# Kernel tuning notes

Hardware: AMD Instinct MI355X
Metric: run time of the kernel (lower is better)

Reference implementation:

```python
import jax, jax.numpy as jnp
import numpy as np

FIELD_DIMS = [26000] * 39
EMBED_DIM = 64
MLP_DIMS = [400, 400, 400]
BATCH = 16384
OFFSETS = jnp.asarray(np.concatenate(([0], np.cumsum(FIELD_DIMS)[:-1])), dtype=jnp.int32)
BN_INV = 1.0 / np.sqrt(1.0 + 1e-5)  # eval-mode BatchNorm1d: running_mean=0, running_var=1


def setup_inputs() -> dict:
    key = jax.random.key(0)
    ks = jax.random.split(key, 16)
    B, F, E = BATCH, len(FIELD_DIMS), EMBED_DIM
    V = sum(FIELD_DIMS)
    s = lambda k, shp, sc=0.05: (jax.random.normal(k, shp, jnp.float32) * sc)
    inp = {
        "x": jax.random.randint(ks[0], (B, F), 0, FIELD_DIMS[0], dtype=jnp.int32),
        "emb_table": s(ks[1], (V, E)),
        "lin_table": s(ks[2], (V, 1)),
        "lin_bias": jnp.zeros((1,), jnp.float32),
        "sparse_var": s(ks[3], (F, E), 0.1),
        "Wt": s(ks[4], (F, E, E)),  # per-field Linear weights, (out,in) layout
        "bt": jnp.zeros((F, E), jnp.float32),
    }
    dims = [F * E] + MLP_DIMS
    for i in range(3):
        inp[f"W{i+1}"] = s(ks[5 + i], (dims[i], dims[i + 1]))
        inp[f"b{i+1}"] = jnp.zeros((dims[i + 1],), jnp.float32)
        inp[f"g{i+1}"] = jnp.ones((dims[i + 1],), jnp.float32)
        inp[f"be{i+1}"] = jnp.zeros((dims[i + 1],), jnp.float32)
    inp["Wout"] = s(ks[9], (MLP_DIMS[-1], 1))
    inp["bout"] = jnp.zeros((1,), jnp.float32)
    return inp


def reference(x, emb_table, lin_table, lin_bias, sparse_var, Wt, bt,
              W1, b1, g1, be1, W2, b2, g2, be2, W3, b3, g3, be3, Wout, bout):
    B = x.shape[0]
    idx = x + OFFSETS[None, :]                       # (B, F) global vocab ids
    # sparse gate (detached in torch), eval-mode hard threshold mask
    sv = jax.nn.sigmoid(jax.lax.stop_gradient(sparse_var) * 15.0)
    sv = jnp.where(sv > 0.001, sv, 0.0)              # (F, E)
    embed_x = emb_table[idx] * sv                    # (B, F, E) gather + gate
    # per-field small Linear, batched as one einsum (torch: y = e @ W.T + b)
    trans = jnp.einsum('bfi,foi->bfo', embed_x, Wt) + bt  # (B, F, E)
    # FM second-order term
    sum_f = trans.sum(axis=1)                        # (B, E)
    fm = 0.5 * jnp.sum(sum_f * sum_f - (trans * trans).sum(axis=1),
                       axis=-1, keepdims=True)       # (B, 1)
    # first-order linear term
    lin = lin_table[idx].sum(axis=1) + lin_bias      # (B, 1)
    # MLP on flattened gated embeddings (Linear -> BN(eval) -> ReLU)
    h = embed_x.reshape(B, -1)
    for W, b, g, be in ((W1, b1, g1, be1), (W2, b2, g2, be2), (W3, b3, g3, be3)):
        h = jax.nn.relu((h @ W + b) * (BN_INV * g) + be)
    mlp = h @ Wout + bout                            # (B, 1)
    return jax.nn.sigmoid(jnp.squeeze(lin + fm + mlp, axis=1))  # (B,)
```

## Files before the change

kernel.cpp:

```cpp
#include <hip/hip_runtime.h>

#define BT 16384
#define NF 39
#define FD 26000

typedef unsigned short u16;
typedef unsigned int u32;
typedef short bf16x8 __attribute__((ext_vector_type(8)));
typedef float f32x4 __attribute__((ext_vector_type(4)));

__device__ __forceinline__ float bf2f(u16 h) {
  union { u32 u; float f; } v; v.u = ((u32)h) << 16; return v.f;
}
__device__ __forceinline__ u16 f2bf(float f) {
  union { float f; u32 u; } v; v.f = f;
  u32 r = v.u + 0x7fffu + ((v.u >> 16) & 1u);
  return (u16)(r >> 16);
}
__device__ __forceinline__ void gld16(const u16* g, u16* l) {
  __builtin_amdgcn_global_load_lds(
      (const __attribute__((address_space(1))) void*)g,
      (__attribute__((address_space(3))) void*)l, 16, 0, 0);
}

__global__ __launch_bounds__(256) void k_prep(
    const float* __restrict__ W1, u16* __restrict__ W1T,
    const float* __restrict__ W2, u16* __restrict__ W2T,
    const float* __restrict__ W3, u16* __restrict__ W3T,
    const float* __restrict__ Wt, u16* __restrict__ Wtb)
{
  int z = blockIdx.z;
  if (z == 3) {
    int idx = (blockIdx.y * 14 + blockIdx.x) * 256 + threadIdx.x;
    if (idx < NF * 4096) Wtb[idx] = f2bf(Wt[idx]);
    return;
  }
  const float* in = (z == 0) ? W1 : (z == 1) ? W2 : W3;
  u16* outp = (z == 0) ? W1T : (z == 1) ? W2T : W3T;
  int K = (z == 0) ? 2496 : 400;
  int Kpad = (z == 0) ? 2496 : 448;
  int r0 = blockIdx.y * 32, c0 = blockIdx.x * 32;
  if (r0 >= Kpad) return;
  __shared__ u16 t[32][33];
  int tx = threadIdx.x & 31, ty = threadIdx.x >> 5;
  for (int i = ty; i < 32; i += 8) {
    int r = r0 + i, c = c0 + tx;
    t[i][tx] = (r < K && c < 400) ? f2bf(in[(long)r * 400 + c]) : (u16)0;
  }
  __syncthreads();
  int r = r0 + tx;
  if (r < Kpad)
    for (int i = ty; i < 32; i += 8)
      outp[(long)(c0 + i) * Kpad + r] = t[tx][i];
}

__global__ __launch_bounds__(256) void k_embed(
    const int* __restrict__ x, const float* __restrict__ emb,
    const float* __restrict__ lin_table, const float* __restrict__ lin_bias,
    const float* __restrict__ sparse_var, const u16* __restrict__ Wtb,
    const float* __restrict__ bt, u16* __restrict__ h0, float* __restrict__ base)
{
  __shared__ u16                s_x[32 * NF];
  __shared__ float              s_sv[NF * 64];
  __shared__ float              s_bt[NF * 64];
  __shared__ __align__(16) u16  s_emb[2][32 * 72];
  __shared__ __align__(16) u16  s_wt[2][64 * 64];
  __shared__ float              s_fm[64];
  __shared__ float              s_lin[32];

  const int tid = threadIdx.x;
  const int b0 = blockIdx.x * 32;

  for (int i = tid; i < 32 * NF; i += 256) s_x[i] = (u16)x[b0 * NF + i];
  for (int i = tid; i < NF * 64; i += 256) {
    float v = sparse_var[i];
    float s = 1.0f / (1.0f + __expf(-15.0f * v));
    s_sv[i] = (s > 0.001f) ? s : 0.0f;
    s_bt[i] = bt[i];
  }
  __syncthreads();

  const int wave = tid >> 6, lane = tid & 63;
  const int quad = lane >> 4, c16 = lane & 15;
  const int mt = wave & 1, nh = wave >> 1;
  const int g_row = tid >> 3, g_c8 = (tid & 7) * 8;
  const int wrow = lane >> 3;
  const int wchk = (lane & 7) ^ wrow;

  float q[4] = {0.f, 0.f, 0.f, 0.f};
  float accS[2][4] = {{0.f,0.f,0.f,0.f},{0.f,0.f,0.f,0.f}};

  #pragma unroll
  for (int i = 0; i < 2; ++i) {
    int ii = wave * 2 + i;
    gld16(Wtb + (ii * 8 + wrow) * 64 + wchk * 8, &s_wt[0][ii * 512]);
  }
  {
    long gi = (long)((int)s_x[g_row * NF + 0]);
    float4 e0 = *(const float4*)&emb[gi * 64 + g_c8];
    float4 e1 = *(const float4*)&emb[gi * 64 + g_c8 + 4];
    union { uint4 v; u16 h[8]; } p;
    p.h[0] = f2bf(e0.x * s_sv[g_c8 + 0]);
    p.h[1] = f2bf(e0.y * s_sv[g_c8 + 1]);
    p.h[2] = f2bf(e0.z * s_sv[g_c8 + 2]);
    p.h[3] = f2bf(e0.w * s_sv[g_c8 + 3]);
    p.h[4] = f2bf(e1.x * s_sv[g_c8 + 4]);
    p.h[5] = f2bf(e1.y * s_sv[g_c8 + 5]);
    p.h[6] = f2bf(e1.z * s_sv[g_c8 + 6]);
    p.h[7] = f2bf(e1.w * s_sv[g_c8 + 7]);
    *(uint4*)&s_emb[0][g_row * 72 + g_c8] = p.v;
    *(uint4*)&h0[(long)(b0 + g_row) * 2496 + g_c8] = p.v;
  }
  __syncthreads();

  for (int f = 0; f < NF; ++f) {
    const int cur = f & 1, nxt = cur ^ 1;
    float4 e0, e1;
    const bool more = (f + 1) < NF;
    if (more) {
      #pragma unroll
      for (int i = 0; i < 2; ++i) {
        int ii = wave * 2 + i;
        gld16(Wtb + (f + 1) * 4096 + (ii * 8 + wrow) * 64 + wchk * 8,
              &s_wt[nxt][ii * 512]);
      }
      long gi = (long)((int)s_x[g_row * NF + f + 1] + (f + 1) * FD);
      e0 = *(const float4*)&emb[gi * 64 + g_c8];
      e1 = *(const float4*)&emb[gi * 64 + g_c8 + 4];
    }

    bf16x8 a0 = *(const bf16x8*)&s_emb[cur][(mt * 16 + c16) * 72 + quad * 8];
    bf16x8 a1 = *(const bf16x8*)&s_emb[cur][(mt * 16 + c16) * 72 + 32 + quad * 8];
    #pragma unroll
    for (int j = 0; j < 2; ++j) {
      int row = (nh * 2 + j) * 16 + c16;
      int pc0 = quad ^ (row & 7);
      int pc1 = (quad + 4) ^ (row & 7);
      bf16x8 bb0 = *(const bf16x8*)&s_wt[cur][row * 64 + pc0 * 8];
      bf16x8 bb1 = *(const bf16x8*)&s_wt[cur][row * 64 + pc1 * 8];
      f32x4 acc = {0.f, 0.f, 0.f, 0.f};
      acc = __builtin_amdgcn_mfma_f32_16x16x32_bf16(a0, bb0, acc, 0, 0, 0);
      acc = __builtin_amdgcn_mfma_f32_16x16x32_bf16(a1, bb1, acc, 0, 0, 0);
      float btv = s_bt[f * 64 + row];
      #pragma unroll
      for (int r = 0; r < 4; ++r) {
        float t = acc[r] + btv;
        accS[j][r] += t;
        q[r] += t * t;
      }
    }

    if (more) {
      union { uint4 v; u16 h[8]; } p;
      const float* sv = &s_sv[(f + 1) * 64 + g_c8];
      p.h[0] = f2bf(e0.x * sv[0]);
      p.h[1] = f2bf(e0.y * sv[1]);
      p.h[2] = f2bf(e0.z * sv[2]);
      p.h[3] = f2bf(e0.w * sv[3]);
      p.h[4] = f2bf(e1.x * sv[4]);
      p.h[5] = f2bf(e1.y * sv[5]);
      p.h[6] = f2bf(e1.z * sv[6]);
      p.h[7] = f2bf(e1.w * sv[7]);
      *(uint4*)&s_emb[nxt][g_row * 72 + g_c8] = p.v;
      *(uint4*)&h0[(long)(b0 + g_row) * 2496 + (f + 1) * 64 + g_c8] = p.v;
    }
    __syncthreads();
  }

  #pragma unroll
  for (int r = 0; r < 4; ++r) {
    float v = accS[0][r] * accS[0][r] + accS[1][r] * accS[1][r] - q[r];
    v += __shfl_xor(v, 1, 64);
    v += __shfl_xor(v, 2, 64);
    v += __shfl_xor(v, 4, 64);
    v += __shfl_xor(v, 8, 64);
    if (c16 == 0) s_fm[nh * 32 + mt * 16 + quad * 4 + r] = v;
  }
  {
    int row = tid >> 3, fi = tid & 7;
    float lv = 0.f;
    for (int f = fi; f < NF; f += 8)
      lv += lin_table[(int)s_x[row * NF + f] + f * FD];
    lv += __shfl_xor(lv, 1, 64);
    lv += __shfl_xor(lv, 2, 64);
    lv += __shfl_xor(lv, 4, 64);
    if (fi == 0) s_lin[row] = lv;
  }
  __syncthreads();
  if (tid < 32)
    base[b0 + tid] = s_lin[tid] + lin_bias[0]
                   + 0.5f * (s_fm[tid] + s_fm[32 + tid]);
}

__global__ __launch_bounds__(256) void k_gemm(
    const u16* __restrict__ A, int lda, const u16* __restrict__ Bt, int ldb,
    int kit, const float* __restrict__ bias, const float* __restrict__ g,
    const float* __restrict__ be, u16* __restrict__ C, int ldc)
{
  __shared__ __align__(16) u16 sA[128 * 64];
  __shared__ __align__(16) u16 sB[112 * 64];

  const int tid = threadIdx.x;
  int bid = blockIdx.x;
  int xcd = bid & 7;
  int j = bid >> 3;
  const int m0 = (xcd * 16 + (j >> 2)) * 128;
  const int n0 = (j & 3) * 112;

  const int wave = tid >> 6, lane = tid & 63;
  const int quad = lane >> 4, c16 = lane & 15;

  const int srow = lane >> 3;
  const int sclog = (lane & 7) ^ (srow & 7);
  const u16* gA = A + (long)m0 * lda + sclog * 8;
  const u16* gB = Bt + (long)n0 * ldb + sclog * 8;

  f32x4 acc[2][7];
  #pragma unroll
  for (int mtt = 0; mtt < 2; ++mtt)
    #pragma unroll
    for (int nt = 0; nt < 7; ++nt) acc[mtt][nt] = {0.f, 0.f, 0.f, 0.f};

  for (int kk = 0; kk < kit; ++kk) {
    const int k0 = kk * 64;
    #pragma unroll
    for (int it = 0; it < 4; ++it) {
      int s = wave * 4 + it;
      gld16(gA + (long)(s * 8 + srow) * lda + k0, &sA[s * 512]);
    }
    gld16(gB + (long)(wave * 8 + srow) * ldb + k0, &sB[wave * 512]);
    gld16(gB + (long)((wave + 4) * 8 + srow) * ldb + k0, &sB[(wave + 4) * 512]);
    gld16(gB + (long)((wave + 8) * 8 + srow) * ldb + k0, &sB[(wave + 8) * 512]);
    if (wave < 2)
      gld16(gB + (long)((wave + 12) * 8 + srow) * ldb + k0, &sB[(wave + 12) * 512]);
    __syncthreads();

    #pragma unroll
    for (int ks = 0; ks < 2; ++ks) {
      const int co = ((ks * 4 + quad) ^ (c16 & 7)) * 8;
      bf16x8 a0 = *(const bf16x8*)&sA[(wave * 32 + c16) * 64 + co];
      bf16x8 a1 = *(const bf16x8*)&sA[(wave * 32 + 16 + c16) * 64 + co];
      #pragma unroll
      for (int nt = 0; nt < 7; ++nt) {
        bf16x8 b = *(const bf16x8*)&sB[(nt * 16 + c16) * 64 + co];
        acc[0][nt] = __builtin_amdgcn_mfma_f32_16x16x32_bf16(a0, b, acc[0][nt], 0, 0, 0);
        acc[1][nt] = __builtin_amdgcn_mfma_f32_16x16x32_bf16(a1, b, acc[1][nt], 0, 0, 0);
      }
    }
    __syncthreads();
  }

  const float BN_INV = 0.9999950000374997f;
  #pragma unroll
  for (int nt = 0; nt < 7; ++nt) {
    int col = n0 + nt * 16 + c16;
    if (col < 400) {
      float bb = bias[col];
      float sc = BN_INV * g[col];
      float bv = be[col];
      #pragma unroll
      for (int mtt = 0; mtt < 2; ++mtt) {
        #pragma unroll
        for (int r = 0; r < 4; ++r) {
          int row = m0 + wave * 32 + mtt * 16 + quad * 4 + r;
          float y = (acc[mtt][nt][r] + bb) * sc + bv;
          y = fmaxf(y, 0.f);
          C[(long)row * ldc + col] = f2bf(y);
        }
      }
    } else if (col < ldc) {
      #pragma unroll
      for (int mtt = 0; mtt < 2; ++mtt)
        #pragma unroll
        for (int r = 0; r < 4; ++r)
          C[(long)(m0 + wave * 32 + mtt * 16 + quad * 4 + r) * ldc + col] = 0;
    }
  }
}

__global__ __launch_bounds__(256) void k_final(
    const u16* __restrict__ h3, const float* __restrict__ Wout,
    const float* __restrict__ bout, const float* __restrict__ base,
    float* __restrict__ out)
{
  int wave = threadIdx.x >> 6, lane = threadIdx.x & 63;
  int b = blockIdx.x * 4 + wave;
  float s = 0.f;
  for (int jj = lane; jj < 400; jj += 64)
    s += bf2f(h3[(long)b * 448 + jj]) * Wout[jj];
  #pragma unroll
  for (int m = 32; m >= 1; m >>= 1) s += __shfl_xor(s, m, 64);
  if (lane == 0) {
    float z = s + base[b] + bout[0];
    out[b] = 1.0f / (1.0f + __expf(-z));
  }
}

extern "C" void kernel_launch(void* const* d_in, const int* in_sizes, int n_in,
                              void* d_out, int out_size, void* d_ws, size_t ws_size,
                              hipStream_t stream)
{
  const int*   x         = (const int*)d_in[0];
  const float* emb       = (const float*)d_in[1];
  const float* lin_table = (const float*)d_in[2];
  const float* lin_bias  = (const float*)d_in[3];
  const float* svar      = (const float*)d_in[4];
  const float* Wt        = (const float*)d_in[5];
  const float* bt        = (const float*)d_in[6];
  const float* W1  = (const float*)d_in[7];
  const float* b1  = (const float*)d_in[8];
  const float* g1  = (const float*)d_in[9];
  const float* be1 = (const float*)d_in[10];
  const float* W2  = (const float*)d_in[11];
  const float* b2  = (const float*)d_in[12];
  const float* g2  = (const float*)d_in[13];
  const float* be2 = (const float*)d_in[14];
  const float* W3  = (const float*)d_in[15];
  const float* b3  = (const float*)d_in[16];
  const float* g3  = (const float*)d_in[17];
  const float* be3 = (const float*)d_in[18];
  const float* Wo  = (const float*)d_in[19];
  const float* bo  = (const float*)d_in[20];

  char* ws = (char*)d_ws;
  size_t off = 0;
  u16* h0 = (u16*)(ws + off);     off += (size_t)BT * 2496 * 2;
  u16* h1 = (u16*)(ws + off);     off += (size_t)BT * 448 * 2;
  u16* h2 = (u16*)(ws + off);     off += (size_t)BT * 448 * 2;
  u16* h3 = (u16*)(ws + off);     off += (size_t)BT * 448 * 2;
  float* base = (float*)(ws + off); off += (size_t)BT * 4;
  u16* W1T = (u16*)(ws + off);    off += (size_t)448 * 2496 * 2;
  u16* W2T = (u16*)(ws + off);    off += (size_t)448 * 448 * 2;
  u16* W3T = (u16*)(ws + off);    off += (size_t)448 * 448 * 2;
  u16* Wtb = (u16*)(ws + off);    off += (size_t)NF * 4096 * 2;
  (void)ws_size; (void)in_sizes; (void)n_in; (void)out_size;

  k_prep<<<dim3(14, 78, 4), 256, 0, stream>>>(W1, W1T, W2, W2T, W3, W3T, Wt, Wtb);
  k_embed<<<512, 256, 0, stream>>>(x, emb, lin_table, lin_bias, svar, Wtb, bt,
                                   h0, base);
  k_gemm<<<512, 256, 0, stream>>>(h0, 2496, W1T, 2496, 39, b1, g1, be1, h1, 448);
  k_gemm<<<512, 256, 0, stream>>>(h1, 448, W2T, 448, 7, b2, g2, be2, h2, 448);
  k_gemm<<<512, 256, 0, stream>>>(h2, 448, W3T, 448, 7, b3, g3, be3, h3, 448);
  k_final<<<4096, 256, 0, stream>>>(h3, Wo, bo, base, (float*)d_out);
}
```

Before: 473.1 us.

## Split embedding gather into wide-grid kernel and FM kernel reading h0

The fused embed kernel, which serially gathered 39 fields per 32-row block, is split in two. A new gather kernel launches one block per (field, row-tile) so the random embedding reads run with far more parallelism. A separate FM kernel then streams the gated bf16 embeddings back from h0 through async LDS loads, and the sigmoid gate is computed once in the prep kernel. This trades an extra write-then-read of h0 (about 80MB of bf16) and one more launch for better latency hiding on the gather.

```diff
diff --git a/kernel.cpp b/kernel.cpp
--- a/kernel.cpp
+++ b/kernel.cpp
@@ -27,12 +27,18 @@
     const float* __restrict__ W1, u16* __restrict__ W1T,
     const float* __restrict__ W2, u16* __restrict__ W2T,
     const float* __restrict__ W3, u16* __restrict__ W3T,
-    const float* __restrict__ Wt, u16* __restrict__ Wtb)
+    const float* __restrict__ Wt, u16* __restrict__ Wtb,
+    const float* __restrict__ sparse_var, float* __restrict__ svg)
 {
   int z = blockIdx.z;
   if (z == 3) {
     int idx = (blockIdx.y * 14 + blockIdx.x) * 256 + threadIdx.x;
     if (idx < NF * 4096) Wtb[idx] = f2bf(Wt[idx]);
+    if (idx < NF * 64) {
+      float v = sparse_var[idx];
+      float s = 1.0f / (1.0f + __expf(-15.0f * v));
+      svg[idx] = (s > 0.001f) ? s : 0.0f;
+    }
     return;
   }
   const float* in = (z == 0) ? W1 : (z == 1) ? W2 : W3;
@@ -54,16 +60,42 @@
       outp[(long)(c0 + i) * Kpad + r] = t[tx][i];
 }
 
-__global__ __launch_bounds__(256) void k_embed(
+__global__ __launch_bounds__(256) void k_gather(
     const int* __restrict__ x, const float* __restrict__ emb,
-    const float* __restrict__ lin_table, const float* __restrict__ lin_bias,
-    const float* __restrict__ sparse_var, const u16* __restrict__ Wtb,
-    const float* __restrict__ bt, u16* __restrict__ h0, float* __restrict__ base)
+    const float* __restrict__ svg, u16* __restrict__ h0)
+{
+  const int f = blockIdx.x;
+  const int b0 = blockIdx.y * 32;
+  const int tid = threadIdx.x;
+  const int g_row = tid >> 3, g_c8 = (tid & 7) * 8;
+
+  int xv = x[(b0 + g_row) * NF + f];
+  long gi = (long)xv + (long)f * FD;
+  float4 e0 = *(const float4*)&emb[gi * 64 + g_c8];
+  float4 e1 = *(const float4*)&emb[gi * 64 + g_c8 + 4];
+  float4 s0 = *(const float4*)&svg[f * 64 + g_c8];
+  float4 s1 = *(const float4*)&svg[f * 64 + g_c8 + 4];
+  union { uint4 v; u16 h[8]; } p;
+  p.h[0] = f2bf(e0.x * s0.x);
+  p.h[1] = f2bf(e0.y * s0.y);
+  p.h[2] = f2bf(e0.z * s0.z);
+  p.h[3] = f2bf(e0.w * s0.w);
+  p.h[4] = f2bf(e1.x * s1.x);
+  p.h[5] = f2bf(e1.y * s1.y);
+  p.h[6] = f2bf(e1.z * s1.z);
+  p.h[7] = f2bf(e1.w * s1.w);
+  *(uint4*)&h0[(long)(b0 + g_row) * 2496 + f * 64 + g_c8] = p.v;
+}
+
+__global__ __launch_bounds__(256) void k_fm(
+    const int* __restrict__ x, const float* __restrict__ lin_table,
+    const float* __restrict__ lin_bias, const u16* __restrict__ Wtb,
+    const float* __restrict__ bt, const u16* __restrict__ h0,
+    float* __restrict__ base)
 {
   __shared__ u16                s_x[32 * NF];
-  __shared__ float              s_sv[NF * 64];
   __shared__ float              s_bt[NF * 64];
-  __shared__ __align__(16) u16  s_emb[2][32 * 72];
+  __shared__ __align__(16) u16  s_a[2][32 * 64];
   __shared__ __align__(16) u16  s_wt[2][64 * 64];
   __shared__ float              s_fm[64];
   __shared__ float              s_lin[32];
@@ -72,97 +104,64 @@
   const int b0 = blockIdx.x * 32;
 
   for (int i = tid; i < 32 * NF; i += 256) s_x[i] = (u16)x[b0 * NF + i];
-  for (int i = tid; i < NF * 64; i += 256) {
-    float v = sparse_var[i];
-    float s = 1.0f / (1.0f + __expf(-15.0f * v));
-    s_sv[i] = (s > 0.001f) ? s : 0.0f;
-    s_bt[i] = bt[i];
-  }
+  for (int i = tid; i < NF * 64; i += 256) s_bt[i] = bt[i];
   __syncthreads();
 
   const int wave = tid >> 6, lane = tid & 63;
   const int quad = lane >> 4, c16 = lane & 15;
   const int mt = wave & 1, nh = wave >> 1;
-  const int g_row = tid >> 3, g_c8 = (tid & 7) * 8;
-  const int wrow = lane >> 3;
-  const int wchk = (lane & 7) ^ wrow;
+  const int srow = lane >> 3;
+  const int schk = (lane & 7) ^ srow;
+  const u16* gA = h0 + (long)(b0 + wave * 8 + srow) * 2496 + schk * 8;
 
   float q[4] = {0.f, 0.f, 0.f, 0.f};
   float accS[2][4] = {{0.f,0.f,0.f,0.f},{0.f,0.f,0.f,0.f}};
 
+  gld16(gA, &s_a[0][wave * 512]);
   #pragma unroll
   for (int i = 0; i < 2; ++i) {
     int ii = wave * 2 + i;
-    gld16(Wtb + (ii * 8 + wrow) * 64 + wchk * 8, &s_wt[0][ii * 512]);
-  }
-  {
-    long gi = (long)((int)s_x[g_row * NF + 0]);
-    float4 e0 = *(const float4*)&emb[gi * 64 + g_c8];
-    float4 e1 = *(const float4*)&emb[gi * 64 + g_c8 + 4];
-    union { uint4 v; u16 h[8]; } p;
-    p.h[0] = f2bf(e0.x * s_sv[g_c8 + 0]);
-    p.h[1] = f2bf(e0.y * s_sv[g_c8 + 1]);
-    p.h[2] = f2bf(e0.z * s_sv[g_c8 + 2]);
-    p.h[3] = f2bf(e0.w * s_sv[g_c8 + 3]);
-    p.h[4] = f2bf(e1.x * s_sv[g_c8 + 4]);
-    p.h[5] = f2bf(e1.y * s_sv[g_c8 + 5]);
-    p.h[6] = f2bf(e1.z * s_sv[g_c8 + 6]);
-    p.h[7] = f2bf(e1.w * s_sv[g_c8 + 7]);
-    *(uint4*)&s_emb[0][g_row * 72 + g_c8] = p.v;
-    *(uint4*)&h0[(long)(b0 + g_row) * 2496 + g_c8] = p.v;
+    gld16(Wtb + (ii * 8 + srow) * 64 + schk * 8, &s_wt[0][ii * 512]);
   }
   __syncthreads();
 
   for (int f = 0; f < NF; ++f) {
     const int cur = f & 1, nxt = cur ^ 1;
-    float4 e0, e1;
     const bool more = (f + 1) < NF;
     if (more) {
+      gld16(gA + (f + 1) * 64, &s_a[nxt][wave * 512]);
       #pragma unroll
       for (int i = 0; i < 2; ++i) {
         int ii = wave * 2 + i;
-        gld16(Wtb + (f + 1) * 4096 + (ii * 8 + wrow) * 64 + wchk * 8,
+        gld16(Wtb + (f + 1) * 4096 + (ii * 8 + srow) * 64 + schk * 8,
               &s_wt[nxt][ii * 512]);
       }
-      long gi = (long)((int)s_x[g_row * NF + f + 1] + (f + 1) * FD);
-      e0 = *(const float4*)&emb[gi * 64 + g_c8];
-      e1 = *(const float4*)&emb[gi * 64 + g_c8 + 4];
-    }
-
-    bf16x8 a0 = *(const bf16x8*)&s_emb[cur][(mt * 16 + c16) * 72 + quad * 8];
-    bf16x8 a1 = *(const bf16x8*)&s_emb[cur][(mt * 16 + c16) * 72 + 32 + quad * 8];
-    #pragma unroll
-    for (int j = 0; j < 2; ++j) {
-      int row = (nh * 2 + j) * 16 + c16;
-      int pc0 = quad ^ (row & 7);
-      int pc1 = (quad + 4) ^ (row & 7);
-      bf16x8 bb0 = *(const bf16x8*)&s_wt[cur][row * 64 + pc0 * 8];
-      bf16x8 bb1 = *(const bf16x8*)&s_wt[cur][row * 64 + pc1 * 8];
-      f32x4 acc = {0.f, 0.f, 0.f, 0.f};
-      acc = __builtin_amdgcn_mfma_f32_16x16x32_bf16(a0, bb0, acc, 0, 0, 0);
-      acc = __builtin_amdgcn_mfma_f32_16x16x32_bf16(a1, bb1, acc, 0, 0, 0);
-      float btv = s_bt[f * 64 + row];
-      #pragma unroll
-      for (int r = 0; r < 4; ++r) {
-        float t = acc[r] + btv;
-        accS[j][r] += t;
-        q[r] += t * t;
+    }
+
+    {
+      int row = mt * 16 + c16;
+      int pa0 = quad ^ (row & 7);
+      int pa1 = (quad + 4) ^ (row & 7);
+      bf16x8 a0 = *(const bf16x8*)&s_a[cur][row * 64 + pa0 * 8];
+      bf16x8 a1 = *(const bf16x8*)&s_a[cur][row * 64 + pa1 * 8];
+      #pragma unroll
+      for (int j = 0; j < 2; ++j) {
+        int brow = (nh * 2 + j) * 16 + c16;
+        int pb0 = quad ^ (brow & 7);
+        int pb1 = (quad + 4) ^ (brow & 7);
+        bf16x8 bb0 = *(const bf16x8*)&s_wt[cur][brow * 64 + pb0 * 8];
+        bf16x8 bb1 = *(const bf16x8*)&s_wt[cur][brow * 64 + pb1 * 8];
+        f32x4 acc = {0.f, 0.f, 0.f, 0.f};
+        acc = __builtin_amdgcn_mfma_f32_16x16x32_bf16(a0, bb0, acc, 0, 0, 0);
+        acc = __builtin_amdgcn_mfma_f32_16x16x32_bf16(a1, bb1, acc, 0, 0, 0);
+        float btv = s_bt[f * 64 + brow];
+        #pragma unroll
+        for (int r = 0; r < 4; ++r) {
+          float t = acc[r] + btv;
+          accS[j][r] += t;
+          q[r] += t * t;
+        }
       }
-    }
-
-    if (more) {
-      union { uint4 v; u16 h[8]; } p;
-      const float* sv = &s_sv[(f + 1) * 64 + g_c8];
-      p.h[0] = f2bf(e0.x * sv[0]);
-      p.h[1] = f2bf(e0.y * sv[1]);
-      p.h[2] = f2bf(e0.z * sv[2]);
-      p.h[3] = f2bf(e0.w * sv[3]);
-      p.h[4] = f2bf(e1.x * sv[4]);
-      p.h[5] = f2bf(e1.y * sv[5]);
-      p.h[6] = f2bf(e1.z * sv[6]);
-      p.h[7] = f2bf(e1.w * sv[7]);
-      *(uint4*)&s_emb[nxt][g_row * 72 + g_c8] = p.v;
-      *(uint4*)&h0[(long)(b0 + g_row) * 2496 + (f + 1) * 64 + g_c8] = p.v;
     }
     __syncthreads();
   }
@@ -333,11 +332,13 @@
   u16* W2T = (u16*)(ws + off);    off += (size_t)448 * 448 * 2;
   u16* W3T = (u16*)(ws + off);    off += (size_t)448 * 448 * 2;
   u16* Wtb = (u16*)(ws + off);    off += (size_t)NF * 4096 * 2;
+  float* svg = (float*)(ws + off); off += (size_t)NF * 64 * 4;
   (void)ws_size; (void)in_sizes; (void)n_in; (void)out_size;
 
-  k_prep<<<dim3(14, 78, 4), 256, 0, stream>>>(W1, W1T, W2, W2T, W3, W3T, Wt, Wtb);
-  k_embed<<<512, 256, 0, stream>>>(x, emb, lin_table, lin_bias, svar, Wtb, bt,
-                                   h0, base);
+  k_prep<<<dim3(14, 78, 4), 256, 0, stream>>>(W1, W1T, W2, W2T, W3, W3T,
+                                              Wt, Wtb, svar, svg);
+  k_gather<<<dim3(NF, 512), 256, 0, stream>>>(x, emb, svg, h0);
+  k_fm<<<512, 256, 0, stream>>>(x, lin_table, lin_bias, Wtb, bt, h0, base);
   k_gemm<<<512, 256, 0, stream>>>(h0, 2496, W1T, 2496, 39, b1, g1, be1, h1, 448);
   k_gemm<<<512, 256, 0, stream>>>(h1, 448, W2T, 448, 7, b2, g2, be2, h2, 448);
   k_gemm<<<512, 256, 0, stream>>>(h2, 448, W3T, 448, 7, b3, g3, be3, h3, 448);
```

Result: slower. 506.8 us (+7.1%).
